# Optimization experiments

Measured on AMD Instinct MI355X. Metric: run time of the kernel, lower is better.

Reference implementation:

```python
import jax, jax.numpy as jnp
import numpy as np

DIM = 128

def _mlp2(x, W1, b1, W2, b2):
    return jax.nn.relu(x @ W1 + b1) @ W2 + b2

def setup_inputs() -> dict:
    key = jax.random.key(0)
    ks = jax.random.split(key, 16)
    n_var, n_con, n_nodes = 600000, 400000, 1000000
    s2 = 1.0 / np.sqrt(2.0)
    sd = 1.0 / np.sqrt(DIM)
    inp = {
        'var_node_features': jax.random.normal(ks[0], (n_var, 2), jnp.float32),
        'con_node_features': jax.random.normal(ks[1], (n_con, 2), jnp.float32),
        'node_types': jnp.zeros((n_nodes,), jnp.int32),
        'assoc_var': jnp.arange(n_var, dtype=jnp.int64),
        'assoc_con': jnp.arange(n_con, dtype=jnp.int64),
        # var_mlp params
        'vW1': jax.random.uniform(ks[2], (2, DIM), jnp.float32, -s2, s2),
        'vb1': jnp.zeros((DIM,), jnp.float32),
        'vW2': jax.random.uniform(ks[3], (DIM, DIM), jnp.float32, -sd, sd),
        'vb2': jnp.zeros((DIM,), jnp.float32),
        # con_mlp params
        'cW1': jax.random.uniform(ks[4], (2, DIM), jnp.float32, -s2, s2),
        'cb1': jnp.zeros((DIM,), jnp.float32),
        'cW2': jax.random.uniform(ks[5], (DIM, DIM), jnp.float32, -sd, sd),
        'cb2': jnp.zeros((DIM,), jnp.float32),
        # head params fc1..fc4
        'W1': jax.random.uniform(ks[6], (DIM, DIM), jnp.float32, -sd, sd),
        'b1': jnp.zeros((DIM,), jnp.float32),
        'W2': jax.random.uniform(ks[7], (DIM, DIM), jnp.float32, -sd, sd),
        'b2': jnp.zeros((DIM,), jnp.float32),
        'W3': jax.random.uniform(ks[8], (DIM, DIM), jnp.float32, -sd, sd),
        'b3': jnp.zeros((DIM,), jnp.float32),
        'W4': jax.random.uniform(ks[9], (DIM, 1), jnp.float32, -sd, sd),
        'b4': jnp.zeros((1,), jnp.float32),
    }
    return inp

def reference(var_node_features, con_node_features, node_types, assoc_var, assoc_con,
              vW1, vb1, vW2, vb2, cW1, cb1, cW2, cb2,
              W1, b1, W2, b2, W3, b3, W4, b4):
    n = _mlp2(var_node_features, vW1, vb1, vW2, vb2)   # [n_var, dim]
    e = _mlp2(con_node_features, cW1, cb1, cW2, cb2)   # [n_con, dim]
    # scatter into shared node tensor (var first, then con overwrites)
    x = jnp.zeros((node_types.shape[0], n.shape[-1]), n.dtype)
    x = x.at[assoc_var].set(n)
    x = x.at[assoc_con].set(e)
    # gather variable-node embeddings
    x = x[assoc_var]                                   # [n_var, dim]
    x = jax.nn.relu(x @ W1 + b1)  # dropout is identity in eval mode
    x = jax.nn.relu(x @ W2 + b2)
    x = jax.nn.relu(x @ W3 + b3)
    x = jax.nn.sigmoid(x @ W4 + b4)
    return x.squeeze(-1)
```

## Files before the change

### kernel.cpp

```cpp
#include <hip/hip_runtime.h>
#include <hip/hip_bf16.h>

typedef unsigned short u16;
typedef unsigned int u32;
typedef __attribute__((ext_vector_type(8))) short short8;
typedef __attribute__((ext_vector_type(4))) float f32x4;
typedef __attribute__((ext_vector_type(4))) u32 u32x4;

#define MFMA16(a, b, c) __builtin_amdgcn_mfma_f32_16x16x32_bf16((a), (b), (c), 0, 0, 0)
#define S8(v) __builtin_bit_cast(short8, (v))

__device__ __forceinline__ u32 pack2(float a, float b) {
    union { __hip_bfloat162 h; u32 u; } v;
    v.h = __float22bfloat162_rn(make_float2(a, b));
    return v.u;
}
__device__ __forceinline__ u16 f2b(float f) {
    union { float f; u32 i; } v; v.f = f;
    u32 x = v.i;
    return (u16)((x + 0x7FFFu + ((x >> 16) & 1u)) >> 16);
}

__global__ void wt_prep(const float* __restrict__ vW2, const float* __restrict__ cW2,
                        const float* __restrict__ W1f, const float* __restrict__ W2f,
                        const float* __restrict__ W3f, u16* __restrict__ wt) {
    int i = blockIdx.x * 256 + threadIdx.x;
    if (i >= 5 * 16384) return;
    int l = i >> 14, e = i & 16383;
    int fr = e >> 9, lane = (e >> 3) & 63, j = e & 7;
    int ot = fr >> 2, ks = fr & 3;
    int c = lane & 15, q = lane >> 4;
    int f = 32 * ks + 16 * (j >> 2) + 4 * q + (j & 3);
    const float* src = (l == 0) ? vW2 : (l == 1) ? cW2 : (l == 2) ? W1f
                     : (l == 3) ? W2f : W3f;
    wt[i] = f2b(src[f * 128 + ot * 16 + c]);
}


#define PRE_Q(WL, BSRC, QQ, S) do {                                           \
    const u16* _wp = (WL) + (QQ) * 8 * 512 + lane * 8;                        \
    w##S##0 = *(const short8*)(_wp + 0 * 512);                                \
    w##S##1 = *(const short8*)(_wp + 1 * 512);                                \
    w##S##2 = *(const short8*)(_wp + 2 * 512);                                \
    w##S##3 = *(const short8*)(_wp + 3 * 512);                                \
    w##S##4 = *(const short8*)(_wp + 4 * 512);                                \
    w##S##5 = *(const short8*)(_wp + 5 * 512);                                \
    w##S##6 = *(const short8*)(_wp + 6 * 512);                                \
    w##S##7 = *(const short8*)(_wp + 7 * 512);                                \
    biv##S##0 = *(const f32x4*)((BSRC) + ((QQ) * 2 + 0) * 16 + q * 4);        \
    biv##S##1 = *(const f32x4*)((BSRC) + ((QQ) * 2 + 1) * 16 + q * 4);        \
} while (0)

#define CHAIN_MID(W0, W1, W2, W3, BIVV, K0, K1, K2, K3, RELU, OUT, C0, C1)    \
  { f32x4 acc = MFMA16(W0, S8(K0), BIVV);                                     \
    acc = MFMA16(W1, S8(K1), acc);                                            \
    acc = MFMA16(W2, S8(K2), acc);                                            \
    acc = MFMA16(W3, S8(K3), acc);                                            \
    float v0 = acc[0], v1 = acc[1], v2 = acc[2], v3 = acc[3];                 \
    if (RELU) { v0 = fmaxf(v0, 0.f); v1 = fmaxf(v1, 0.f);                     \
                v2 = fmaxf(v2, 0.f); v3 = fmaxf(v3, 0.f); }                   \
    OUT.C0 = pack2(v0, v1); OUT.C1 = pack2(v2, v3); }

#define Q_O(W0, W1, W2, W3, BIVV, I, O, QQ, C0, C1, RELU)                     \
  CHAIN_MID(W0, W1, W2, W3, BIVV, I##_r0_k0, I##_r0_k1, I##_r0_k2, I##_r0_k3, RELU, O##_r0_k##QQ, C0, C1) \
  CHAIN_MID(W0, W1, W2, W3, BIVV, I##_r1_k0, I##_r1_k1, I##_r1_k2, I##_r1_k3, RELU, O##_r1_k##QQ, C0, C1) \
  CHAIN_MID(W0, W1, W2, W3, BIVV, I##_r2_k0, I##_r2_k1, I##_r2_k2, I##_r2_k3, RELU, O##_r2_k##QQ, C0, C1) \
  CHAIN_MID(W0, W1, W2, W3, BIVV, I##_r3_k0, I##_r3_k1, I##_r3_k2, I##_r3_k3, RELU, O##_r3_k##QQ, C0, C1)

#define Q_MID(I, O, QQ, S, RELU)                                              \
  Q_O(w##S##0, w##S##1, w##S##2, w##S##3, biv##S##0, I, O, QQ, x, y, RELU)    \
  Q_O(w##S##4, w##S##5, w##S##6, w##S##7, biv##S##1, I, O, QQ, z, w, RELU)

#define CHAIN_LAST(W0, W1, W2, W3, BIVV, K0, K1, K2, K3, WW, PD)              \
  { f32x4 acc = MFMA16(W0, S8(K0), BIVV);                                     \
    acc = MFMA16(W1, S8(K1), acc);                                            \
    acc = MFMA16(W2, S8(K2), acc);                                            \
    acc = MFMA16(W3, S8(K3), acc);                                            \
    PD += fmaxf(acc[0], 0.f) * WW.x + fmaxf(acc[1], 0.f) * WW.y               \
        + fmaxf(acc[2], 0.f) * WW.z + fmaxf(acc[3], 0.f) * WW.w; }

#define QL_O(W0, W1, W2, W3, BIVV, I, OT)                                     \
  { float4 ww = *(const float4*)(W4 + (OT) * 16 + q * 4);                     \
    CHAIN_LAST(W0, W1, W2, W3, BIVV, I##_r0_k0, I##_r0_k1, I##_r0_k2, I##_r0_k3, ww, pd0) \
    CHAIN_LAST(W0, W1, W2, W3, BIVV, I##_r1_k0, I##_r1_k1, I##_r1_k2, I##_r1_k3, ww, pd1) \
    CHAIN_LAST(W0, W1, W2, W3, BIVV, I##_r2_k0, I##_r2_k1, I##_r2_k2, I##_r2_k3, ww, pd2) \
    CHAIN_LAST(W0, W1, W2, W3, BIVV, I##_r3_k0, I##_r3_k1, I##_r3_k2, I##_r3_k3, ww, pd3) }

#define Q_LAST(I, QQ, S)                                                      \
  QL_O(w##S##0, w##S##1, w##S##2, w##S##3, biv##S##0, I, (QQ) * 2 + 0)        \
  QL_O(w##S##4, w##S##5, w##S##6, w##S##7, biv##S##1, I, (QQ) * 2 + 1)

#define P0_ROW(V, C0, C1, I0, I1)                                             \
  { float x0 = fmaxf(fmaf(I0, wA.x, fmaf(I1, wB.x, bz.x)), 0.f);              \
    float x1 = fmaxf(fmaf(I0, wA.y, fmaf(I1, wB.y, bz.y)), 0.f);              \
    float x2 = fmaxf(fmaf(I0, wA.z, fmaf(I1, wB.z, bz.z)), 0.f);              \
    float x3 = fmaxf(fmaf(I0, wA.w, fmaf(I1, wB.w, bz.w)), 0.f);              \
    V.C0 = pack2(x0, x1); V.C1 = pack2(x2, x3); }

#define P0_HI(KS, HI, C0, C1)                                                 \
  { const int base = (KS) * 32 + (HI) * 16 + q * 4;                           \
    float4 wA = *(const float4*)(w1p + base);                                 \
    float4 wB = *(const float4*)(w1p + 128 + base);                           \
    float4 bz = *(const float4*)(b1p + base);                                 \
    P0_ROW(a_r0_k##KS, C0, C1, in00, in10)                                    \
    P0_ROW(a_r1_k##KS, C0, C1, in01, in11)                                    \
    P0_ROW(a_r2_k##KS, C0, C1, in02, in12)                                    \
    P0_ROW(a_r3_k##KS, C0, C1, in03, in13) }

#define P0_KS(KS) P0_HI(KS, 0, x, y) P0_HI(KS, 1, z, w)

#define P0_IN(RT, I0, I1)                                                     \
  { int g = rowW + (RT) * 16 + c; I0 = 0.f; I1 = 0.f;                         \
    if (g < n_var) { float2 t2 = *(const float2*)(fb + 2 * g); I0 = t2.x; I1 = t2.y; } }

__global__ __attribute__((amdgpu_flat_work_group_size(128, 128),
                          amdgpu_waves_per_eu(2, 2))) void
mlp_fused(
    const float* __restrict__ varf, const float* __restrict__ conf,
    const float* __restrict__ vW1, const float* __restrict__ vb1, const float* __restrict__ vb2,
    const float* __restrict__ cW1, const float* __restrict__ cb1, const float* __restrict__ cb2,
    const float* __restrict__ b1,  const float* __restrict__ b2,  const float* __restrict__ b3,
    const float* __restrict__ W4,  const float* __restrict__ b4,
    const u16* __restrict__ WT,   float* __restrict__ out,
    int n_var, int n_con)
{
    const int t = threadIdx.x;
    const int lane = t & 63, wv = t >> 6;
    const int c = lane & 15, q = lane >> 4;
    const int row0 = blockIdx.x * 128;
    const int rowW = row0 + wv * 64;
    const bool use_con = (row0 < n_con);

    u32x4 a_r0_k0, a_r0_k1, a_r0_k2, a_r0_k3;
    u32x4 a_r1_k0, a_r1_k1, a_r1_k2, a_r1_k3;
    u32x4 a_r2_k0, a_r2_k1, a_r2_k2, a_r2_k3;
    u32x4 a_r3_k0, a_r3_k1, a_r3_k2, a_r3_k3;
    u32x4 b_r0_k0, b_r0_k1, b_r0_k2, b_r0_k3;
    u32x4 b_r1_k0, b_r1_k1, b_r1_k2, b_r1_k3;
    u32x4 b_r2_k0, b_r2_k1, b_r2_k2, b_r2_k3;
    u32x4 b_r3_k0, b_r3_k1, b_r3_k2, b_r3_k3;
    short8 wu0, wu1, wu2, wu3, wu4, wu5, wu6, wu7;
    short8 wv0, wv1, wv2, wv3, wv4, wv5, wv6, wv7;
    f32x4 bivu0, bivu1, bivv0, bivv1;

    const u16* WL0 = WT + (size_t)16384 * (use_con ? 1 : 0);
    const u16* WL1 = WT + (size_t)16384 * 2;
    const u16* WL2 = WT + (size_t)16384 * 3;
    const u16* WL3 = WT + (size_t)16384 * 4;
    const float* bs0 = use_con ? cb2 : vb2;

    PRE_Q(WL0, bs0, 0, u);

    {
        const float* w1p = use_con ? cW1 : vW1;
        const float* b1p = use_con ? cb1 : vb1;
        const float* fb  = use_con ? conf : varf;
        float in00, in01, in02, in03, in10, in11, in12, in13;
        P0_IN(0, in00, in10) P0_IN(1, in01, in11)
        P0_IN(2, in02, in12) P0_IN(3, in03, in13)
        P0_KS(0) P0_KS(1) P0_KS(2) P0_KS(3)
    }

    float pd0 = 0.f, pd1 = 0.f, pd2 = 0.f, pd3 = 0.f;

    PRE_Q(WL0, bs0, 1, v);  Q_MID(a, b, 0, u, 0)
    PRE_Q(WL0, bs0, 2, u);  Q_MID(a, b, 1, v, 0)
    PRE_Q(WL0, bs0, 3, v);  Q_MID(a, b, 2, u, 0)
    PRE_Q(WL1, b1,  0, u);  Q_MID(a, b, 3, v, 0)
    PRE_Q(WL1, b1,  1, v);  Q_MID(b, a, 0, u, 1)
    PRE_Q(WL1, b1,  2, u);  Q_MID(b, a, 1, v, 1)
    PRE_Q(WL1, b1,  3, v);  Q_MID(b, a, 2, u, 1)
    PRE_Q(WL2, b2,  0, u);  Q_MID(b, a, 3, v, 1)
    PRE_Q(WL2, b2,  1, v);  Q_MID(a, b, 0, u, 1)
    PRE_Q(WL2, b2,  2, u);  Q_MID(a, b, 1, v, 1)
    PRE_Q(WL2, b2,  3, v);  Q_MID(a, b, 2, u, 1)
    PRE_Q(WL3, b3,  0, u);  Q_MID(a, b, 3, v, 1)
    PRE_Q(WL3, b3,  1, v);  Q_LAST(b, 0, u)
    PRE_Q(WL3, b3,  2, u);  Q_LAST(b, 1, v)
    PRE_Q(WL3, b3,  3, v);  Q_LAST(b, 2, u)
                            Q_LAST(b, 3, v)

    float bias4 = b4[0];
#define REDUCE(PD, RT)                                                        \
    { float v = PD;                                                           \
      v += __shfl_xor(v, 16);                                                 \
      v += __shfl_xor(v, 32);                                                 \
      if (q == 0) {                                                           \
          int g = rowW + (RT) * 16 + c;                                       \
          if (g < n_var) out[g] = 1.f / (1.f + __expf(-(v + bias4)));         \
      } }
    REDUCE(pd0, 0) REDUCE(pd1, 1) REDUCE(pd2, 2) REDUCE(pd3, 3)
#undef REDUCE
}

extern "C" void kernel_launch(void* const* d_in, const int* in_sizes, int n_in,
                              void* d_out, int out_size, void* d_ws, size_t ws_size,
                              hipStream_t stream) {
    const float* varf = (const float*)d_in[0];
    const float* conf = (const float*)d_in[1];
    const float* vW1 = (const float*)d_in[5];
    const float* vb1 = (const float*)d_in[6];
    const float* vW2 = (const float*)d_in[7];
    const float* vb2 = (const float*)d_in[8];
    const float* cW1 = (const float*)d_in[9];
    const float* cb1 = (const float*)d_in[10];
    const float* cW2 = (const float*)d_in[11];
    const float* cb2 = (const float*)d_in[12];
    const float* W1  = (const float*)d_in[13];
    const float* b1  = (const float*)d_in[14];
    const float* W2  = (const float*)d_in[15];
    const float* b2  = (const float*)d_in[16];
    const float* W3  = (const float*)d_in[17];
    const float* b3  = (const float*)d_in[18];
    const float* W4  = (const float*)d_in[19];
    const float* b4  = (const float*)d_in[20];

    int n_var = in_sizes[0] / 2;
    int n_con = in_sizes[1] / 2;
    u16* wt = (u16*)d_ws;

    hipLaunchKernelGGL(wt_prep, dim3(320), dim3(256), 0, stream,
                       vW2, cW2, W1, W2, W3, wt);

    int nb = (n_var + 127) / 128;
    hipLaunchKernelGGL(mlp_fused, dim3(nb), dim3(128), 0, stream,
                       varf, conf, vW1, vb1, vb2, cW1, cb1, cb2,
                       b1, b2, b3, W4, b4, wt, (float*)d_out, n_var, n_con);
}
```

Measured before the change: 178.0 us.

## Stage bf16 weights in LDS with double-buffered async loads and 512-thread blocks

Each block now copies each layer's pre-swizzled bf16 weight matrix from global memory into a double-buffered LDS area using global_load_lds. Biases and W4 are also staged into LDS, and all waves in the block read the shared copy instead of each wave streaming the weights from global memory. Blocks grow to 512 threads with 32 rows per wave, and the grid is split so blocks never straddle the con/var boundary. The aim is to cut redundant per-wave weight traffic through L1/L2. The cost is a large LDS footprint, extra block-wide barriers, and half the rows per wave, which gives less reuse of each weight fragment loaded into registers.

```diff
diff --git a/kernel.cpp b/kernel.cpp
--- a/kernel.cpp
+++ b/kernel.cpp
@@ -9,6 +9,7 @@
 
 #define MFMA16(a, b, c) __builtin_amdgcn_mfma_f32_16x16x32_bf16((a), (b), (c), 0, 0, 0)
 #define S8(v) __builtin_bit_cast(short8, (v))
+#define SBAR() __builtin_amdgcn_sched_barrier(0)
 
 __device__ __forceinline__ u32 pack2(float a, float b) {
     union { __hip_bfloat162 h; u32 u; } v;
@@ -19,6 +20,12 @@
     union { float f; u32 i; } v; v.f = f;
     u32 x = v.i;
     return (u16)((x + 0x7FFFu + ((x >> 16) & 1u)) >> 16);
+}
+
+__device__ __forceinline__ void gl_lds16(const u16* g, u16* l) {
+    __builtin_amdgcn_global_load_lds(
+        (const __attribute__((address_space(1))) void*)g,
+        (__attribute__((address_space(3))) void*)l, 16, 0, 0);
 }
 
 __global__ void wt_prep(const float* __restrict__ vW2, const float* __restrict__ cW2,
@@ -37,58 +44,90 @@
 }
 
 
-#define PRE_Q(WL, BSRC, QQ, S) do {                                           \
-    const u16* _wp = (WL) + (QQ) * 8 * 512 + lane * 8;                        \
-    w##S##0 = *(const short8*)(_wp + 0 * 512);                                \
-    w##S##1 = *(const short8*)(_wp + 1 * 512);                                \
-    w##S##2 = *(const short8*)(_wp + 2 * 512);                                \
-    w##S##3 = *(const short8*)(_wp + 3 * 512);                                \
-    w##S##4 = *(const short8*)(_wp + 4 * 512);                                \
-    w##S##5 = *(const short8*)(_wp + 5 * 512);                                \
-    w##S##6 = *(const short8*)(_wp + 6 * 512);                                \
-    w##S##7 = *(const short8*)(_wp + 7 * 512);                                \
-    biv##S##0 = *(const f32x4*)((BSRC) + ((QQ) * 2 + 0) * 16 + q * 4);        \
-    biv##S##1 = *(const f32x4*)((BSRC) + ((QQ) * 2 + 1) * 16 + q * 4);        \
-} while (0)
-
-#define CHAIN_MID(W0, W1, W2, W3, BIVV, K0, K1, K2, K3, RELU, OUT, C0, C1)    \
-  { f32x4 acc = MFMA16(W0, S8(K0), BIVV);                                     \
-    acc = MFMA16(W1, S8(K1), acc);                                            \
-    acc = MFMA16(W2, S8(K2), acc);                                            \
-    acc = MFMA16(W3, S8(K3), acc);                                            \
-    float v0 = acc[0], v1 = acc[1], v2 = acc[2], v3 = acc[3];                 \
+#define STAGE(LSRC, B) do {                                                   \
+    _Pragma("unroll")                                                         \
+    for (int r = 0; r < 4; ++r) {                                             \
+        int ch = r * 8 + wv;                                                  \
+        gl_lds16(WT + (size_t)(LSRC) * 16384 + ch * 512 + lane * 8,           \
+                 ldsw + (B) * 16384 + ch * 512);                              \
+    } } while (0)
+
+#define LDSH(B, QQ, H) do {                                                   \
+    const u16* _lp = ldsw + (B) * 16384 + ((QQ) * 8 + (H) * 2) * 512 + lane * 8; \
+    wu0 = *(const short8*)(_lp + 0 * 512);                                    \
+    wu1 = *(const short8*)(_lp + 1 * 512);                                    \
+    wu2 = *(const short8*)(_lp + 4 * 512);                                    \
+    wu3 = *(const short8*)(_lp + 5 * 512);                                    \
+} while (0)
+
+#define BIVL(LB, QQ) do {                                                     \
+    biv0 = *(const f32x4*)(ldsb + (LB) * 128 + ((QQ) * 2 + 0) * 16 + q * 4);  \
+    biv1 = *(const f32x4*)(ldsb + (LB) * 128 + ((QQ) * 2 + 1) * 16 + q * 4);  \
+} while (0)
+
+#define HALF0(I) do {                                                         \
+    ac00 = MFMA16(wu0, S8(I##_r0_k0), biv0);                                  \
+    ac01 = MFMA16(wu0, S8(I##_r1_k0), biv0);                                  \
+    ac10 = MFMA16(wu2, S8(I##_r0_k0), biv1);                                  \
+    ac11 = MFMA16(wu2, S8(I##_r1_k0), biv1);                                  \
+    ac00 = MFMA16(wu1, S8(I##_r0_k1), ac00);                                  \
+    ac01 = MFMA16(wu1, S8(I##_r1_k1), ac01);                                  \
+    ac10 = MFMA16(wu3, S8(I##_r0_k1), ac10);                                  \
+    ac11 = MFMA16(wu3, S8(I##_r1_k1), ac11);                                  \
+} while (0)
+
+#define HALF1(I) do {                                                         \
+    ac00 = MFMA16(wu0, S8(I##_r0_k2), ac00);                                  \
+    ac01 = MFMA16(wu0, S8(I##_r1_k2), ac01);                                  \
+    ac10 = MFMA16(wu2, S8(I##_r0_k2), ac10);                                  \
+    ac11 = MFMA16(wu2, S8(I##_r1_k2), ac11);                                  \
+    ac00 = MFMA16(wu1, S8(I##_r0_k3), ac00);                                  \
+    ac01 = MFMA16(wu1, S8(I##_r1_k3), ac01);                                  \
+    ac10 = MFMA16(wu3, S8(I##_r0_k3), ac10);                                  \
+    ac11 = MFMA16(wu3, S8(I##_r1_k3), ac11);                                  \
+} while (0)
+
+#define EPI(RELU, ACC, OUT, C0, C1)                                           \
+  { float v0 = ACC[0], v1 = ACC[1], v2 = ACC[2], v3 = ACC[3];                 \
     if (RELU) { v0 = fmaxf(v0, 0.f); v1 = fmaxf(v1, 0.f);                     \
                 v2 = fmaxf(v2, 0.f); v3 = fmaxf(v3, 0.f); }                   \
     OUT.C0 = pack2(v0, v1); OUT.C1 = pack2(v2, v3); }
 
-#define Q_O(W0, W1, W2, W3, BIVV, I, O, QQ, C0, C1, RELU)                     \
-  CHAIN_MID(W0, W1, W2, W3, BIVV, I##_r0_k0, I##_r0_k1, I##_r0_k2, I##_r0_k3, RELU, O##_r0_k##QQ, C0, C1) \
-  CHAIN_MID(W0, W1, W2, W3, BIVV, I##_r1_k0, I##_r1_k1, I##_r1_k2, I##_r1_k3, RELU, O##_r1_k##QQ, C0, C1) \
-  CHAIN_MID(W0, W1, W2, W3, BIVV, I##_r2_k0, I##_r2_k1, I##_r2_k2, I##_r2_k3, RELU, O##_r2_k##QQ, C0, C1) \
-  CHAIN_MID(W0, W1, W2, W3, BIVV, I##_r3_k0, I##_r3_k1, I##_r3_k2, I##_r3_k3, RELU, O##_r3_k##QQ, C0, C1)
-
-#define Q_MID(I, O, QQ, S, RELU)                                              \
-  Q_O(w##S##0, w##S##1, w##S##2, w##S##3, biv##S##0, I, O, QQ, x, y, RELU)    \
-  Q_O(w##S##4, w##S##5, w##S##6, w##S##7, biv##S##1, I, O, QQ, z, w, RELU)
-
-#define CHAIN_LAST(W0, W1, W2, W3, BIVV, K0, K1, K2, K3, WW, PD)              \
-  { f32x4 acc = MFMA16(W0, S8(K0), BIVV);                                     \
-    acc = MFMA16(W1, S8(K1), acc);                                            \
-    acc = MFMA16(W2, S8(K2), acc);                                            \
-    acc = MFMA16(W3, S8(K3), acc);                                            \
-    PD += fmaxf(acc[0], 0.f) * WW.x + fmaxf(acc[1], 0.f) * WW.y               \
-        + fmaxf(acc[2], 0.f) * WW.z + fmaxf(acc[3], 0.f) * WW.w; }
-
-#define QL_O(W0, W1, W2, W3, BIVV, I, OT)                                     \
-  { float4 ww = *(const float4*)(W4 + (OT) * 16 + q * 4);                     \
-    CHAIN_LAST(W0, W1, W2, W3, BIVV, I##_r0_k0, I##_r0_k1, I##_r0_k2, I##_r0_k3, ww, pd0) \
-    CHAIN_LAST(W0, W1, W2, W3, BIVV, I##_r1_k0, I##_r1_k1, I##_r1_k2, I##_r1_k3, ww, pd1) \
-    CHAIN_LAST(W0, W1, W2, W3, BIVV, I##_r2_k0, I##_r2_k1, I##_r2_k2, I##_r2_k3, ww, pd2) \
-    CHAIN_LAST(W0, W1, W2, W3, BIVV, I##_r3_k0, I##_r3_k1, I##_r3_k2, I##_r3_k3, ww, pd3) }
-
-#define Q_LAST(I, QQ, S)                                                      \
-  QL_O(w##S##0, w##S##1, w##S##2, w##S##3, biv##S##0, I, (QQ) * 2 + 0)        \
-  QL_O(w##S##4, w##S##5, w##S##6, w##S##7, biv##S##1, I, (QQ) * 2 + 1)
+#define QUARTER(B, LB, I, O, QQ, RELU) do {                                   \
+    BIVL(LB, QQ);                                                             \
+    LDSH(B, QQ, 0);                                                           \
+    HALF0(I);                                                                 \
+    LDSH(B, QQ, 1);                                                           \
+    HALF1(I);                                                                 \
+    EPI(RELU, ac00, O##_r0_k##QQ, x, y)                                       \
+    EPI(RELU, ac01, O##_r1_k##QQ, x, y)                                       \
+    EPI(RELU, ac10, O##_r0_k##QQ, z, w)                                       \
+    EPI(RELU, ac11, O##_r1_k##QQ, z, w)                                       \
+} while (0)
+
+#define LAYER(B, LB, I, O, RELU)                                              \
+    QUARTER(B, LB, I, O, 0, RELU);                                            \
+    QUARTER(B, LB, I, O, 1, RELU);                                            \
+    QUARTER(B, LB, I, O, 2, RELU);                                            \
+    QUARTER(B, LB, I, O, 3, RELU);
+
+#define QUARTER_LAST(B, I, QQ) do {                                           \
+    BIVL(3, QQ);                                                              \
+    f32x4 ww0 = *(const f32x4*)(ldsb + 512 + ((QQ) * 2 + 0) * 16 + q * 4);    \
+    f32x4 ww1 = *(const f32x4*)(ldsb + 512 + ((QQ) * 2 + 1) * 16 + q * 4);    \
+    LDSH(B, QQ, 0);                                                           \
+    HALF0(I);                                                                 \
+    LDSH(B, QQ, 1);                                                           \
+    HALF1(I);                                                                 \
+    pd0 += fmaxf(ac00[0], 0.f) * ww0[0] + fmaxf(ac00[1], 0.f) * ww0[1]        \
+         + fmaxf(ac00[2], 0.f) * ww0[2] + fmaxf(ac00[3], 0.f) * ww0[3];       \
+    pd0 += fmaxf(ac10[0], 0.f) * ww1[0] + fmaxf(ac10[1], 0.f) * ww1[1]        \
+         + fmaxf(ac10[2], 0.f) * ww1[2] + fmaxf(ac10[3], 0.f) * ww1[3];       \
+    pd1 += fmaxf(ac01[0], 0.f) * ww0[0] + fmaxf(ac01[1], 0.f) * ww0[1]        \
+         + fmaxf(ac01[2], 0.f) * ww0[2] + fmaxf(ac01[3], 0.f) * ww0[3];       \
+    pd1 += fmaxf(ac11[0], 0.f) * ww1[0] + fmaxf(ac11[1], 0.f) * ww1[1]        \
+         + fmaxf(ac11[2], 0.f) * ww1[2] + fmaxf(ac11[3], 0.f) * ww1[3];       \
+} while (0)
 
 #define P0_ROW(V, C0, C1, I0, I1)                                             \
   { float x0 = fmaxf(fmaf(I0, wA.x, fmaf(I1, wB.x, bz.x)), 0.f);              \
@@ -103,18 +142,16 @@
     float4 wB = *(const float4*)(w1p + 128 + base);                           \
     float4 bz = *(const float4*)(b1p + base);                                 \
     P0_ROW(a_r0_k##KS, C0, C1, in00, in10)                                    \
-    P0_ROW(a_r1_k##KS, C0, C1, in01, in11)                                    \
-    P0_ROW(a_r2_k##KS, C0, C1, in02, in12)                                    \
-    P0_ROW(a_r3_k##KS, C0, C1, in03, in13) }
+    P0_ROW(a_r1_k##KS, C0, C1, in01, in11) }
 
 #define P0_KS(KS) P0_HI(KS, 0, x, y) P0_HI(KS, 1, z, w)
 
 #define P0_IN(RT, I0, I1)                                                     \
   { int g = rowW + (RT) * 16 + c; I0 = 0.f; I1 = 0.f;                         \
-    if (g < n_var) { float2 t2 = *(const float2*)(fb + 2 * g); I0 = t2.x; I1 = t2.y; } }
-
-__global__ __attribute__((amdgpu_flat_work_group_size(128, 128),
-                          amdgpu_waves_per_eu(2, 2))) void
+    if (g < limit) { float2 t2 = *(const float2*)(fb + 2 * g); I0 = t2.x; I1 = t2.y; } }
+
+__global__ __attribute__((amdgpu_flat_work_group_size(512, 512),
+                          amdgpu_waves_per_eu(4))) void
 mlp_fused(
     const float* __restrict__ varf, const float* __restrict__ conf,
     const float* __restrict__ vW1, const float* __restrict__ vb1, const float* __restrict__ vb2,
@@ -122,63 +159,69 @@
     const float* __restrict__ b1,  const float* __restrict__ b2,  const float* __restrict__ b3,
     const float* __restrict__ W4,  const float* __restrict__ b4,
     const u16* __restrict__ WT,   float* __restrict__ out,
-    int n_var, int n_con)
+    int n_var, int n_con, int nb_con)
 {
     const int t = threadIdx.x;
     const int lane = t & 63, wv = t >> 6;
     const int c = lane & 15, q = lane >> 4;
-    const int row0 = blockIdx.x * 128;
-    const int rowW = row0 + wv * 64;
-    const bool use_con = (row0 < n_con);
+    const int bid = blockIdx.x;
+    const bool use_con = (bid < nb_con);
+    const int row0 = use_con ? bid * 256 : n_con + (bid - nb_con) * 256;
+    const int rowW = row0 + wv * 32;
+    const int limit = use_con ? n_con : n_var;
+
+    __shared__ u16 ldsw[2 * 16384];
+    __shared__ float ldsb[640];
 
     u32x4 a_r0_k0, a_r0_k1, a_r0_k2, a_r0_k3;
     u32x4 a_r1_k0, a_r1_k1, a_r1_k2, a_r1_k3;
-    u32x4 a_r2_k0, a_r2_k1, a_r2_k2, a_r2_k3;
-    u32x4 a_r3_k0, a_r3_k1, a_r3_k2, a_r3_k3;
     u32x4 b_r0_k0, b_r0_k1, b_r0_k2, b_r0_k3;
     u32x4 b_r1_k0, b_r1_k1, b_r1_k2, b_r1_k3;
-    u32x4 b_r2_k0, b_r2_k1, b_r2_k2, b_r2_k3;
-    u32x4 b_r3_k0, b_r3_k1, b_r3_k2, b_r3_k3;
-    short8 wu0, wu1, wu2, wu3, wu4, wu5, wu6, wu7;
-    short8 wv0, wv1, wv2, wv3, wv4, wv5, wv6, wv7;
-    f32x4 bivu0, bivu1, bivv0, bivv1;
-
-    const u16* WL0 = WT + (size_t)16384 * (use_con ? 1 : 0);
-    const u16* WL1 = WT + (size_t)16384 * 2;
-    const u16* WL2 = WT + (size_t)16384 * 3;
-    const u16* WL3 = WT + (size_t)16384 * 4;
+    short8 wu0, wu1, wu2, wu3;
+    f32x4 biv0, biv1;
+    f32x4 ac00, ac01, ac10, ac11;
+
     const float* bs0 = use_con ? cb2 : vb2;
 
-    PRE_Q(WL0, bs0, 0, u);
+    STAGE((use_con ? 1 : 0), 0);
+    STAGE(2, 1);
+    {
+        int which = t >> 7, idx = t & 127;
+        const float* p = (which == 0) ? bs0 : (which == 1) ? b1
+                       : (which == 2) ? b2 : b3;
+        ldsb[t >= 512 ? 0 : t] = (t >= 512) ? ldsb[0] : p[idx];
+        if (t < 128) ldsb[512 + t] = W4[t];
+    }
+    SBAR();
 
     {
         const float* w1p = use_con ? cW1 : vW1;
         const float* b1p = use_con ? cb1 : vb1;
         const float* fb  = use_con ? conf : varf;
-        float in00, in01, in02, in03, in10, in11, in12, in13;
+        float in00, in01, in10, in11;
         P0_IN(0, in00, in10) P0_IN(1, in01, in11)
-        P0_IN(2, in02, in12) P0_IN(3, in03, in13)
         P0_KS(0) P0_KS(1) P0_KS(2) P0_KS(3)
     }
 
-    float pd0 = 0.f, pd1 = 0.f, pd2 = 0.f, pd3 = 0.f;
-
-    PRE_Q(WL0, bs0, 1, v);  Q_MID(a, b, 0, u, 0)
-    PRE_Q(WL0, bs0, 2, u);  Q_MID(a, b, 1, v, 0)
-    PRE_Q(WL0, bs0, 3, v);  Q_MID(a, b, 2, u, 0)
-    PRE_Q(WL1, b1,  0, u);  Q_MID(a, b, 3, v, 0)
-    PRE_Q(WL1, b1,  1, v);  Q_MID(b, a, 0, u, 1)
-    PRE_Q(WL1, b1,  2, u);  Q_MID(b, a, 1, v, 1)
-    PRE_Q(WL1, b1,  3, v);  Q_MID(b, a, 2, u, 1)
-    PRE_Q(WL2, b2,  0, u);  Q_MID(b, a, 3, v, 1)
-    PRE_Q(WL2, b2,  1, v);  Q_MID(a, b, 0, u, 1)
-    PRE_Q(WL2, b2,  2, u);  Q_MID(a, b, 1, v, 1)
-    PRE_Q(WL2, b2,  3, v);  Q_MID(a, b, 2, u, 1)
-    PRE_Q(WL3, b3,  0, u);  Q_MID(a, b, 3, v, 1)
-    PRE_Q(WL3, b3,  1, v);  Q_LAST(b, 0, u)
-    PRE_Q(WL3, b3,  2, u);  Q_LAST(b, 1, v)
-    PRE_Q(WL3, b3,  3, v);  Q_LAST(b, 2, u)
-                            Q_LAST(b, 3, v)
+    float pd0 = 0.f, pd1 = 0.f;
+
+    __syncthreads();
+
+    LAYER(0, 0, a, b, 0)
+    __syncthreads();
+    STAGE(3, 0);  SBAR();
+
+    LAYER(1, 1, b, a, 1)
+    __syncthreads();
+    STAGE(4, 1);  SBAR();
+
+    LAYER(0, 2, a, b, 1)
+    __syncthreads();
+
+    QUARTER_LAST(1, b, 0);
+    QUARTER_LAST(1, b, 1);
+    QUARTER_LAST(1, b, 2);
+    QUARTER_LAST(1, b, 3);
 
     float bias4 = b4[0];
 #define REDUCE(PD, RT)                                                        \
@@ -187,9 +230,9 @@
       v += __shfl_xor(v, 32);                                                 \
       if (q == 0) {                                                           \
           int g = rowW + (RT) * 16 + c;                                       \
-          if (g < n_var) out[g] = 1.f / (1.f + __expf(-(v + bias4)));         \
+          if (g < limit) out[g] = 1.f / (1.f + __expf(-(v + bias4)));         \
       } }
-    REDUCE(pd0, 0) REDUCE(pd1, 1) REDUCE(pd2, 2) REDUCE(pd3, 3)
+    REDUCE(pd0, 0) REDUCE(pd1, 1)
 #undef REDUCE
 }
 
@@ -222,8 +265,10 @@
     hipLaunchKernelGGL(wt_prep, dim3(320), dim3(256), 0, stream,
                        vW2, cW2, W1, W2, W3, wt);
 
-    int nb = (n_var + 127) / 128;
-    hipLaunchKernelGGL(mlp_fused, dim3(nb), dim3(128), 0, stream,
+    int nb_con = (n_con + 255) / 256;
+    int nb_var = (n_var - n_con + 255) / 256;
+    hipLaunchKernelGGL(mlp_fused, dim3(nb_con + nb_var), dim3(512), 0, stream,
                        varf, conf, vW1, vb1, vb2, cW1, cb1, cb2,
-                       b1, b2, b3, W4, b4, wt, (float*)d_out, n_var, n_con);
-}
+                       b1, b2, b3, W4, b4, wt, (float*)d_out, n_var, n_con,
+                       nb_con);
+}
```

New measurement: 177.0 us. About the same (-0.6%).
